# Optimization experiments

Measured on AMD Instinct MI355X. Metric: run time of the kernel, lower is better.

## Reference

```python
import jax, jax.numpy as jnp
import numpy as np

N = 100000   # nodes
E = 256000   # edges
EMB = 300    # emb_dim
L = 5        # num_layer
NUM_BOND_TYPE = 6
NUM_BOND_DIR = 3
BN_EPS = 1e-5


def _bn(h, g, b):
    # BatchNorm1d forward with batch stats (training-mode math, biased var)
    m = jnp.mean(h, axis=0)
    v = jnp.var(h, axis=0)
    return g * (h - m) * jax.lax.rsqrt(v + BN_EPS) + b


def setup_inputs() -> dict:
    key = jax.random.key(0)
    ks = jax.random.split(key, 8)
    x = jax.random.normal(ks[0], (N, EMB), jnp.float32)
    edge_index = jax.random.randint(ks[1], (2, E), 0, N, jnp.int32)
    edge_attr = jax.random.randint(ks[2], (E, 2), 0, 3, jnp.int32)
    # per-layer stacked parameters
    W_bond = jax.random.normal(ks[3], (L, EMB, NUM_BOND_TYPE + NUM_BOND_DIR), jnp.float32) * 0.1
    eps = jnp.zeros((L,), jnp.float32)
    W1 = jax.random.normal(ks[4], (L, 2 * EMB, EMB), jnp.float32) * 0.05
    b1 = jnp.zeros((L, 2 * EMB), jnp.float32)
    bn1_g = jnp.ones((L, 2 * EMB), jnp.float32)
    bn1_b = jnp.zeros((L, 2 * EMB), jnp.float32)
    W2 = jax.random.normal(ks[5], (L, EMB, 2 * EMB), jnp.float32) * 0.05
    b2 = jnp.zeros((L, EMB), jnp.float32)
    bn_g = jnp.ones((L, EMB), jnp.float32)
    bn_b = jnp.zeros((L, EMB), jnp.float32)
    return {"x": x, "W_bond": W_bond, "eps": eps, "W1": W1, "b1": b1,
            "bn1_g": bn1_g, "bn1_b": bn1_b, "W2": W2, "b2": b2,
            "bn_g": bn_g, "bn_b": bn_b,
            "edge_index": edge_index, "edge_attr": edge_attr}


def reference(x, W_bond, eps, W1, b1, bn1_g, bn1_b, W2, b2, bn_g, bn_b,
              edge_index, edge_attr):
    src, dst = edge_index[0], edge_index[1]
    ea0, ea1 = edge_attr[:, 0], edge_attr[:, 1]
    h = x
    for l in range(L):
        # MixedBondEncoder (2-column int branch): two embedding lookups on W.T
        tab = W_bond[l].T  # [9, EMB]
        e = tab[:NUM_BOND_TYPE][ea0] + tab[NUM_BOND_TYPE:][ea1]  # [E, EMB]
        # GIN message: relu(x_j + edge_emb), scatter-add to dst
        msg = jax.nn.relu(h[src] + e)
        agg = jax.ops.segment_sum(msg, dst, num_segments=N)  # [N, EMB]
        z = (1.0 + eps[l]) * h + agg
        # mlp: Linear -> BN -> ReLU -> Linear
        z = z @ W1[l].T + b1[l]
        z = jax.nn.relu(_bn(z, bn1_g[l], bn1_b[l]))
        z = z @ W2[l].T + b2[l]
        # outer BatchNorm, relu except last layer (dropout p=0)
        z = _bn(z, bn_g[l], bn_b[l])
        if l < L - 1:
            z = jax.nn.relu(z)
        h = z
    return h  # JK='last'
```

## Files before the change

kernel.cpp:

```cpp
#include <hip/hip_runtime.h>
#include <hip/hip_bf16.h>
#include <stdint.h>
#include <stddef.h>
#include <string.h>

#define NN 100000
#define NE 256000
#define EMBD 300
#define C1D 600
#define NL 5
#define BNEPS 1e-5f

#define REPBLK 1800

typedef short bf16x8 __attribute__((ext_vector_type(8)));
typedef float f32x4 __attribute__((ext_vector_type(4)));

__device__ __forceinline__ float bf2f(unsigned short u) {
  unsigned int x = ((unsigned int)u) << 16;
  return __uint_as_float(x);
}
__device__ __forceinline__ unsigned short f2bf(float f) {
  unsigned int x = __float_as_uint(f);
  unsigned int r = x + 0x7fffu + ((x >> 16) & 1u);
  return (unsigned short)(r >> 16);
}

__device__ __forceinline__ void split2(float a, float b, unsigned int& hi, unsigned int& lo) {
  float2 p = make_float2(a, b);
  __hip_bfloat162 hb = __float22bfloat162_rn(p);
  unsigned int hraw;
  memcpy(&hraw, &hb, 4);
  float2 hf = __bfloat1622float2(hb);
  float2 lf = make_float2(a - hf.x, b - hf.y);
  __hip_bfloat162 lb = __float22bfloat162_rn(lf);
  unsigned int lraw;
  memcpy(&lraw, &lb, 4);
  hi = hraw; lo = lraw;
}


__global__ void zero_stats_k(float* __restrict__ statrep, int n) {
  int i = blockIdx.x * blockDim.x + threadIdx.x;
  int stride = gridDim.x * blockDim.x;
  for (; i < n; i += stride) statrep[i] = 0.0f;
}

__global__ void preset_ident_k(float* __restrict__ wsf) {
  for (int i = threadIdx.x; i < 300; i += blockDim.x) {
    wsf[1200 + i] = 1.0f;
    wsf[1500 + i] = 0.0f;
  }
}

__global__ void init_agg_k(const float* __restrict__ zin, const float* __restrict__ sc,
                           const float* __restrict__ sh, const float* __restrict__ eps,
                           int l, int relu, float* __restrict__ agg) {
  float s = 1.0f + eps[l];
  int i = blockIdx.x * blockDim.x + threadIdx.x;
  const int n4 = NN * (EMBD / 4);
  if (i >= n4) return;
  int c4 = (i % (EMBD / 4)) * 4;
  float4 v = ((const float4*)zin)[i];
  float4 a = *(const float4*)(sc + c4);
  float4 b = *(const float4*)(sh + c4);
  v.x = v.x * a.x + b.x;
  v.y = v.y * a.y + b.y;
  v.z = v.z * a.z + b.z;
  v.w = v.w * a.w + b.w;
  if (relu) {
    v.x = fmaxf(v.x, 0.0f); v.y = fmaxf(v.y, 0.0f);
    v.z = fmaxf(v.z, 0.0f); v.w = fmaxf(v.w, 0.0f);
  }
  v.x *= s; v.y *= s; v.z *= s; v.w *= s;
  ((float4*)agg)[i] = v;
}

__global__ void edge_scatter_k(const float* __restrict__ zin, const float* __restrict__ Wb_l,
                               const float* __restrict__ sc, const float* __restrict__ sh,
                               int relu,
                               const int* __restrict__ ei, const int* __restrict__ ea,
                               float* __restrict__ agg) {
  __shared__ float tab[EMBD * 9];
  __shared__ float scs[EMBD];
  __shared__ float shs[EMBD];
  for (int i = threadIdx.x; i < EMBD * 9; i += blockDim.x) tab[i] = Wb_l[i];
  for (int i = threadIdx.x; i < EMBD; i += blockDim.x) { scs[i] = sc[i]; shs[i] = sh[i]; }
  __syncthreads();
  int wave = threadIdx.x >> 6;
  int lane = threadIdx.x & 63;
  int e = blockIdx.x * 4 + wave;
  if (e >= NE) return;
  int src = ei[e];
  int dst = ei[NE + e];
  int t0 = ea[2 * e];
  int t1 = ea[2 * e + 1] + 6;
  const float* zs = zin + (size_t)src * EMBD;
  float* ad = agg + (size_t)dst * EMBD;
  for (int d = lane; d < EMBD; d += 64) {
    float hv = zs[d] * scs[d] + shs[d];
    if (relu) hv = fmaxf(hv, 0.0f);
    float m = hv + tab[d * 9 + t0] + tab[d * 9 + t1];
    if (m > 0.0f) atomicAdd(&ad[d], m);
  }
}

__global__ void split_agg_k(unsigned int* __restrict__ a) {
  int i = blockIdx.x * blockDim.x + threadIdx.x;
  const int n4 = NN * (EMBD / 4);
  if (i >= n4) return;
  float4 v = ((const float4*)a)[i];
  unsigned int h0, l0, h1, l1;
  split2(v.x, v.y, h0, l0);
  split2(v.z, v.w, h1, l1);
  uint4 o;
  o.x = __builtin_amdgcn_perm(l0, h0, 0x05040100u);
  o.y = __builtin_amdgcn_perm(l0, h0, 0x07060302u);
  o.z = __builtin_amdgcn_perm(l1, h1, 0x05040100u);
  o.w = __builtin_amdgcn_perm(l1, h1, 0x07060302u);
  ((uint4*)a)[i] = o;
}

__global__ void finalize_k(const float* __restrict__ statrep, int off_sum, int off_sq,
                           int nrep,
                           const float* __restrict__ g, const float* __restrict__ b,
                           float* __restrict__ scale, float* __restrict__ shift, int C) {
  int j = blockIdx.x * blockDim.x + threadIdx.x;
  if (j >= C) return;
  float s = 0.0f, q = 0.0f;
  for (int r = 0; r < nrep; ++r) {
    const float* p = statrep + (size_t)r * REPBLK;
    s += p[off_sum + j];
    q += p[off_sq + j];
  }
  float mean = s * (1.0f / NN);
  float var = q * (1.0f / NN) - mean * mean;
  float sc = g[j] * rsqrtf(var + BNEPS);
  scale[j] = sc;
  shift[j] = b[j] - mean * sc;
}

__global__ void bn_apply_k(const float* __restrict__ z2, const float* __restrict__ scale,
                           const float* __restrict__ shift, int do_relu, float* __restrict__ out) {
  int i = blockIdx.x * blockDim.x + threadIdx.x;
  const int n4 = NN * (EMBD / 4);
  if (i >= n4) return;
  int c4 = (i % (EMBD / 4)) * 4;
  float4 v = ((const float4*)z2)[i];
  float4 sc = *(const float4*)(scale + c4);
  float4 sh = *(const float4*)(shift + c4);
  v.x = v.x * sc.x + sh.x;
  v.y = v.y * sc.y + sh.y;
  v.z = v.z * sc.z + sh.z;
  v.w = v.w * sc.w + sh.w;
  if (do_relu) {
    v.x = fmaxf(v.x, 0.0f); v.y = fmaxf(v.y, 0.0f);
    v.z = fmaxf(v.z, 0.0f); v.w = fmaxf(v.w, 0.0f);
  }
  ((float4*)out)[i] = v;
}


#define TM 128
#define TN 128
#define TK 32
#define LDT 40
#define OTS 136

__global__ __launch_bounds__(256, 2) void gemm1_mfma_k(
    const unsigned int* __restrict__ A,
    const float* __restrict__ W,
    const float* __restrict__ bias,
    unsigned short* __restrict__ Z1,
    float* __restrict__ statrep, int repmask) {
  const int M = NN, K = EMBD, NC = C1D;
  __shared__ unsigned short SM[20480];
  unsigned short* Ah = SM;
  unsigned short* Al = SM + 5120;
  unsigned short* Bh = SM + 10240;
  unsigned short* Bl = SM + 15360;
  unsigned short* OT = SM;

  int tid = threadIdx.x;
  int m0 = blockIdx.x * TM, n0 = blockIdx.y * TN;
  int w = tid >> 6, lane = tid & 63;
  int wm = w & 1, wn = w >> 1;
  int lm16 = lane & 15, quad = lane >> 4;

  f32x4 acc[4][4] = {};

  for (int k0 = 0; k0 < K; k0 += TK) {
#pragma unroll
    for (int i = 0; i < 4; ++i) {
      int u = tid + i * 256;
      int row = u >> 3, q = u & 7;
      int k = k0 + q * 4;
      int m = m0 + row;
      uint4 x = make_uint4(0, 0, 0, 0);
      if (m < M && k + 3 < K) x = *(const uint4*)(A + (size_t)m * K + k);
      unsigned int h01 = __builtin_amdgcn_perm(x.y, x.x, 0x05040100u);
      unsigned int l01 = __builtin_amdgcn_perm(x.y, x.x, 0x07060302u);
      unsigned int h23 = __builtin_amdgcn_perm(x.w, x.z, 0x05040100u);
      unsigned int l23 = __builtin_amdgcn_perm(x.w, x.z, 0x07060302u);
      *(uint2*)&Ah[row * LDT + q * 4] = make_uint2(h01, h23);
      *(uint2*)&Al[row * LDT + q * 4] = make_uint2(l01, l23);
    }
#pragma unroll
    for (int i = 0; i < 4; ++i) {
      int u = tid + i * 256;
      int row = u >> 3, q = u & 7;
      int k = k0 + q * 4;
      int n = n0 + row;
      float4 v = make_float4(0, 0, 0, 0);
      if (n < NC && k + 3 < K) v = *(const float4*)(W + (size_t)n * K + k);
      unsigned int h0, l0, h1, l1;
      split2(v.x, v.y, h0, l0);
      split2(v.z, v.w, h1, l1);
      *(uint2*)&Bh[row * LDT + q * 4] = make_uint2(h0, h1);
      *(uint2*)&Bl[row * LDT + q * 4] = make_uint2(l0, l1);
    }
    __syncthreads();

    bf16x8 ah[4], al[4], bh[4], bl[4];
#pragma unroll
    for (int t = 0; t < 4; ++t) {
      int ar = (wm * 64 + t * 16 + lm16) * LDT + quad * 8;
      ah[t] = *(const bf16x8*)&Ah[ar];
      al[t] = *(const bf16x8*)&Al[ar];
      int br = (wn * 64 + t * 16 + lm16) * LDT + quad * 8;
      bh[t] = *(const bf16x8*)&Bh[br];
      bl[t] = *(const bf16x8*)&Bl[br];
    }
#pragma unroll
    for (int mt = 0; mt < 4; ++mt)
#pragma unroll
      for (int nt = 0; nt < 4; ++nt) {
        acc[mt][nt] = __builtin_amdgcn_mfma_f32_16x16x32_bf16(ah[mt], bh[nt], acc[mt][nt], 0, 0, 0);
        acc[mt][nt] = __builtin_amdgcn_mfma_f32_16x16x32_bf16(al[mt], bh[nt], acc[mt][nt], 0, 0, 0);
        acc[mt][nt] = __builtin_amdgcn_mfma_f32_16x16x32_bf16(ah[mt], bl[nt], acc[mt][nt], 0, 0, 0);
      }
    __syncthreads();
  }

  float* srep = statrep + (size_t)(blockIdx.x & repmask) * REPBLK;

#pragma unroll
  for (int nt = 0; nt < 4; ++nt) {
    int c = n0 + wn * 64 + nt * 16 + lm16;
    bool cv = c < NC;
    float bs = cv ? bias[c] : 0.0f;
    int ocol = wn * 64 + nt * 16 + lm16;
    float csum = 0.0f, csq = 0.0f;
#pragma unroll
    for (int mt = 0; mt < 4; ++mt) {
      int rbase = m0 + wm * 64 + mt * 16 + quad * 4;
      int orow = wm * 64 + mt * 16 + quad * 4;
#pragma unroll
      for (int r = 0; r < 4; ++r) {
        float v = acc[mt][nt][r] + bs;
        OT[(orow + r) * OTS + ocol] = f2bf(v);
        if ((rbase + r) < M && cv) { csum += v; csq += v * v; }
      }
    }
    csum += __shfl_down(csum, 16); csum += __shfl_down(csum, 32);
    csq  += __shfl_down(csq, 16);  csq  += __shfl_down(csq, 32);
    if (quad == 0 && cv) {
      atomicAdd(&srep[c], csum);
      atomicAdd(&srep[600 + c], csq);
    }
  }
  __syncthreads();

  {
    int ncols = NC - n0; if (ncols > TN) ncols = TN;
    int nchunk = ncols >> 3;
    int cc = tid & 15;
    int rr0 = tid >> 4;
    if (cc < nchunk) {
#pragma unroll
      for (int i = 0; i < 8; ++i) {
        int rr = rr0 + i * 16;
        int mm = m0 + rr;
        if (mm < M) {
          uint4 vv = *(const uint4*)&OT[rr * OTS + cc * 8];
          *(uint4*)&Z1[(size_t)mm * NC + n0 + cc * 8] = vv;
        }
      }
    }
  }
}

__global__ __launch_bounds__(256, 2) void gemm2_mfma_k(
    const unsigned short* __restrict__ Z1,
    const float* __restrict__ scale1, const float* __restrict__ shift1,
    const float* __restrict__ W,
    const float* __restrict__ bias,
    float* __restrict__ Z2,
    float* __restrict__ statrep, int repmask) {
  const int M = NN, K = C1D, NC = EMBD;
  __shared__ unsigned short Ah[TM * LDT], Al[TM * LDT];
  __shared__ unsigned short Bh[TN * LDT], Bl[TN * LDT];

  int tid = threadIdx.x;
  int m0 = blockIdx.x * TM, n0 = blockIdx.y * TN;
  int w = tid >> 6, lane = tid & 63;
  int wm = w & 1, wn = w >> 1;
  int lm16 = lane & 15, quad = lane >> 4;

  f32x4 acc[4][4] = {};

  for (int k0 = 0; k0 < K; k0 += TK) {
#pragma unroll
    for (int i = 0; i < 2; ++i) {
      int u = tid + i * 256;
      int row = u >> 2, g = u & 3;
      int k = k0 + g * 8;
      int m = m0 + row;
      float vals[8];
#pragma unroll
      for (int j = 0; j < 8; ++j) vals[j] = 0.0f;
      if (m < M) {
        if (k + 7 < K) {
          union { uint4 u4; unsigned short us[8]; } rr;
          rr.u4 = *(const uint4*)(Z1 + (size_t)m * K + k);
          float4 sc0 = *(const float4*)(scale1 + k);
          float4 sc1 = *(const float4*)(scale1 + k + 4);
          float4 sh0 = *(const float4*)(shift1 + k);
          float4 sh1 = *(const float4*)(shift1 + k + 4);
          const float* scp = &sc0.x; const float* shp = &sh0.x;
          const float* scq = &sc1.x; const float* shq = &sh1.x;
#pragma unroll
          for (int j = 0; j < 4; ++j) {
            vals[j]     = fmaxf(bf2f(rr.us[j])     * scp[j] + shp[j], 0.0f);
            vals[j + 4] = fmaxf(bf2f(rr.us[j + 4]) * scq[j] + shq[j], 0.0f);
          }
        } else {
#pragma unroll
          for (int j = 0; j < 8; ++j) {
            int kk = k + j;
            if (kk < K)
              vals[j] = fmaxf(bf2f(Z1[(size_t)m * K + kk]) * scale1[kk] + shift1[kk], 0.0f);
          }
        }
      }
      unsigned int h[4], l[4];
      split2(vals[0], vals[1], h[0], l[0]);
      split2(vals[2], vals[3], h[1], l[1]);
      split2(vals[4], vals[5], h[2], l[2]);
      split2(vals[6], vals[7], h[3], l[3]);
      *(uint4*)&Ah[row * LDT + g * 8] = make_uint4(h[0], h[1], h[2], h[3]);
      *(uint4*)&Al[row * LDT + g * 8] = make_uint4(l[0], l[1], l[2], l[3]);
    }
#pragma unroll
    for (int i = 0; i < 4; ++i) {
      int u = tid + i * 256;
      int row = u >> 3, q = u & 7;
      int k = k0 + q * 4;
      int n = n0 + row;
      float4 v = make_float4(0, 0, 0, 0);
      if (n < NC) {
        if (k + 3 < K) v = *(const float4*)(W + (size_t)n * K + k);
        else {
          float* vv = &v.x;
#pragma unroll
          for (int j = 0; j < 4; ++j) if (k + j < K) vv[j] = W[(size_t)n * K + k + j];
        }
      }
      unsigned int h0, l0, h1, l1;
      split2(v.x, v.y, h0, l0);
      split2(v.z, v.w, h1, l1);
      *(uint2*)&Bh[row * LDT + q * 4] = make_uint2(h0, h1);
      *(uint2*)&Bl[row * LDT + q * 4] = make_uint2(l0, l1);
    }
    __syncthreads();

    bf16x8 ah[4], al[4], bh[4], bl[4];
#pragma unroll
    for (int t = 0; t < 4; ++t) {
      int ar = (wm * 64 + t * 16 + lm16) * LDT + quad * 8;
      ah[t] = *(const bf16x8*)&Ah[ar];
      al[t] = *(const bf16x8*)&Al[ar];
      int br = (wn * 64 + t * 16 + lm16) * LDT + quad * 8;
      bh[t] = *(const bf16x8*)&Bh[br];
      bl[t] = *(const bf16x8*)&Bl[br];
    }
#pragma unroll
    for (int mt = 0; mt < 4; ++mt)
#pragma unroll
      for (int nt = 0; nt < 4; ++nt) {
        acc[mt][nt] = __builtin_amdgcn_mfma_f32_16x16x32_bf16(ah[mt], bh[nt], acc[mt][nt], 0, 0, 0);
        acc[mt][nt] = __builtin_amdgcn_mfma_f32_16x16x32_bf16(al[mt], bh[nt], acc[mt][nt], 0, 0, 0);
        acc[mt][nt] = __builtin_amdgcn_mfma_f32_16x16x32_bf16(ah[mt], bl[nt], acc[mt][nt], 0, 0, 0);
      }
    __syncthreads();
  }

  float* srep = statrep + (size_t)(blockIdx.x & repmask) * REPBLK;

#pragma unroll
  for (int nt = 0; nt < 4; ++nt) {
    int c = n0 + wn * 64 + nt * 16 + lm16;
    bool cv = c < NC;
    float bs = cv ? bias[c] : 0.0f;
    float csum = 0.0f, csq = 0.0f;
#pragma unroll
    for (int mt = 0; mt < 4; ++mt) {
      int rbase = m0 + wm * 64 + mt * 16 + quad * 4;
#pragma unroll
      for (int r = 0; r < 4; ++r) {
        int mm = rbase + r;
        if (mm < M && cv) {
          float v = acc[mt][nt][r] + bs;
          Z2[(size_t)mm * NC + c] = v;
          csum += v; csq += v * v;
        }
      }
    }
    csum += __shfl_down(csum, 16); csum += __shfl_down(csum, 32);
    csq  += __shfl_down(csq, 16);  csq  += __shfl_down(csq, 32);
    if (quad == 0 && cv) {
      atomicAdd(&srep[1200 + c], csum);
      atomicAdd(&srep[1500 + c], csq);
    }
  }
}


extern "C" void kernel_launch(void* const* d_in, const int* in_sizes, int n_in,
                              void* d_out, int out_size, void* d_ws, size_t ws_size,
                              hipStream_t stream) {
  const float* x    = (const float*)d_in[0];
  const float* Wb   = (const float*)d_in[1];
  const float* eps  = (const float*)d_in[2];
  const float* W1   = (const float*)d_in[3];
  const float* b1   = (const float*)d_in[4];
  const float* bn1g = (const float*)d_in[5];
  const float* bn1b = (const float*)d_in[6];
  const float* W2   = (const float*)d_in[7];
  const float* b2   = (const float*)d_in[8];
  const float* bng  = (const float*)d_in[9];
  const float* bnb  = (const float*)d_in[10];
  const int*   ei   = (const int*)d_in[11];
  const int*   ea   = (const int*)d_in[12];

  float* WS  = (float*)d_ws;
  float* OUT = (float*)d_out;
  float* wsf = (float*)d_ws + (size_t)NN * EMBD;
  float* statrep = wsf + 1800;

  size_t need64 = ((size_t)NN * EMBD + 1800 + (size_t)64 * REPBLK) * sizeof(float);
  int nrep = (ws_size >= need64) ? 64 : 1;
  int repmask = nrep - 1;
  int zn = nrep * REPBLK;

  const int n4 = NN * (EMBD / 4);
  const int eltGrid = (n4 + 255) / 256;

  dim3 g1((NN + TM - 1) / TM, (C1D + TN - 1) / TN);
  dim3 g2((NN + TM - 1) / TM, (EMBD + TN - 1) / TN);

  preset_ident_k<<<1, 256, 0, stream>>>(wsf);

  for (int l = 0; l < NL; ++l) {
    float* aggp = (l & 1) ? OUT : WS;
    float* z1p  = (l & 1) ? WS  : OUT;
    const float* zin = (l == 0) ? x : (const float*)z1p;
    int relu_in = (l > 0) ? 1 : 0;

    zero_stats_k<<<64, 256, 0, stream>>>(statrep, zn);
    init_agg_k<<<eltGrid, 256, 0, stream>>>(zin, wsf + 1200, wsf + 1500, eps, l, relu_in, aggp);
    edge_scatter_k<<<NE / 4, 256, 0, stream>>>(zin, Wb + (size_t)l * EMBD * 9,
                                               wsf + 1200, wsf + 1500, relu_in, ei, ea, aggp);
    split_agg_k<<<eltGrid, 256, 0, stream>>>((unsigned int*)aggp);
    gemm1_mfma_k<<<g1, 256, 0, stream>>>(
        (const unsigned int*)aggp, W1 + (size_t)l * C1D * EMBD, b1 + (size_t)l * C1D,
        (unsigned short*)z1p, statrep, repmask);
    finalize_k<<<3, 256, 0, stream>>>(statrep, 0, 600, nrep, bn1g + (size_t)l * C1D,
                                      bn1b + (size_t)l * C1D, wsf + 0, wsf + 600, C1D);
    gemm2_mfma_k<<<g2, 256, 0, stream>>>(
        (const unsigned short*)z1p, wsf + 0, wsf + 600,
        W2 + (size_t)l * EMBD * C1D, b2 + (size_t)l * EMBD,
        aggp, statrep, repmask);
    finalize_k<<<2, 256, 0, stream>>>(statrep, 1200, 1500, nrep, bng + (size_t)l * EMBD,
                                      bnb + (size_t)l * EMBD, wsf + 1200, wsf + 1500, EMBD);
  }
  bn_apply_k<<<eltGrid, 256, 0, stream>>>(WS, wsf + 1200, wsf + 1500, 0, OUT);
}
```

Measured before the change: 5.341 ms.

## Prefetch next K-tile into registers and swizzle GEMM blocks across XCDs

Both MFMA GEMM kernels now load the next K tile of A and W into registers while the current tile is being multiplied, so global-load latency overlaps with compute. Block indices are also remapped so that blocks sharing an M tile land on the same XCD, which is meant to improve L2 reuse. The remainder-handling branches in gemm2 are simplified because K is divisible by 8. The extra prefetch registers may raise register pressure under the two-blocks-per-CU launch bound.

```diff
diff --git a/kernel.cpp b/kernel.cpp
--- a/kernel.cpp
+++ b/kernel.cpp
@@ -37,6 +37,17 @@
   unsigned int lraw;
   memcpy(&lraw, &lb, 4);
   hi = hraw; lo = lraw;
+}
+
+__device__ __forceinline__ void swizzle_xy(int GX, int GY, int& tx, int& ty) {
+  int nwg = GX * GY;
+  int bid = blockIdx.y * GX + blockIdx.x;
+  int xcd = bid & 7, local = bid >> 3;
+  int q = nwg >> 3, r = nwg & 7;
+  int swz = (xcd < r) ? (xcd * (q + 1) + local)
+                      : (r * (q + 1) + (xcd - r) * q + local);
+  tx = swz / GY;
+  ty = swz - tx * GY;
 }
 
 
@@ -182,44 +193,66 @@
   unsigned short* OT = SM;
 
   int tid = threadIdx.x;
-  int m0 = blockIdx.x * TM, n0 = blockIdx.y * TN;
+  int tx, ty;
+  swizzle_xy(gridDim.x, gridDim.y, tx, ty);
+  int m0 = tx * TM, n0 = ty * TN;
   int w = tid >> 6, lane = tid & 63;
   int wm = w & 1, wn = w >> 1;
   int lm16 = lane & 15, quad = lane >> 4;
+  int srow = tid >> 3, sq = tid & 7;
 
   f32x4 acc[4][4] = {};
+  uint4 pA[4];
+  float4 pB[4];
+
+#pragma unroll
+  for (int i = 0; i < 4; ++i) {
+    int row = srow + i * 32;
+    int k = sq * 4;
+    int m = m0 + row, n = n0 + row;
+    uint4 xa = make_uint4(0, 0, 0, 0);
+    if (m < M && k + 3 < K) xa = *(const uint4*)(A + (size_t)m * K + k);
+    pA[i] = xa;
+    float4 vb = make_float4(0, 0, 0, 0);
+    if (n < NC && k + 3 < K) vb = *(const float4*)(W + (size_t)n * K + k);
+    pB[i] = vb;
+  }
 
   for (int k0 = 0; k0 < K; k0 += TK) {
 #pragma unroll
     for (int i = 0; i < 4; ++i) {
-      int u = tid + i * 256;
-      int row = u >> 3, q = u & 7;
-      int k = k0 + q * 4;
-      int m = m0 + row;
-      uint4 x = make_uint4(0, 0, 0, 0);
-      if (m < M && k + 3 < K) x = *(const uint4*)(A + (size_t)m * K + k);
+      int row = srow + i * 32;
+      uint4 x = pA[i];
       unsigned int h01 = __builtin_amdgcn_perm(x.y, x.x, 0x05040100u);
       unsigned int l01 = __builtin_amdgcn_perm(x.y, x.x, 0x07060302u);
       unsigned int h23 = __builtin_amdgcn_perm(x.w, x.z, 0x05040100u);
       unsigned int l23 = __builtin_amdgcn_perm(x.w, x.z, 0x07060302u);
-      *(uint2*)&Ah[row * LDT + q * 4] = make_uint2(h01, h23);
-      *(uint2*)&Al[row * LDT + q * 4] = make_uint2(l01, l23);
-    }
-#pragma unroll
-    for (int i = 0; i < 4; ++i) {
-      int u = tid + i * 256;
-      int row = u >> 3, q = u & 7;
-      int k = k0 + q * 4;
-      int n = n0 + row;
-      float4 v = make_float4(0, 0, 0, 0);
-      if (n < NC && k + 3 < K) v = *(const float4*)(W + (size_t)n * K + k);
-      unsigned int h0, l0, h1, l1;
-      split2(v.x, v.y, h0, l0);
-      split2(v.z, v.w, h1, l1);
-      *(uint2*)&Bh[row * LDT + q * 4] = make_uint2(h0, h1);
-      *(uint2*)&Bl[row * LDT + q * 4] = make_uint2(l0, l1);
+      *(uint2*)&Ah[row * LDT + sq * 4] = make_uint2(h01, h23);
+      *(uint2*)&Al[row * LDT + sq * 4] = make_uint2(l01, l23);
+      float4 v = pB[i];
+      unsigned int bh0, bl0, bh1, bl1;
+      split2(v.x, v.y, bh0, bl0);
+      split2(v.z, v.w, bh1, bl1);
+      *(uint2*)&Bh[row * LDT + sq * 4] = make_uint2(bh0, bh1);
+      *(uint2*)&Bl[row * LDT + sq * 4] = make_uint2(bl0, bl1);
     }
     __syncthreads();
+
+    if (k0 + TK < K) {
+      int kn = k0 + TK;
+#pragma unroll
+      for (int i = 0; i < 4; ++i) {
+        int row = srow + i * 32;
+        int k = kn + sq * 4;
+        int m = m0 + row, n = n0 + row;
+        uint4 xa = make_uint4(0, 0, 0, 0);
+        if (m < M && k + 3 < K) xa = *(const uint4*)(A + (size_t)m * K + k);
+        pA[i] = xa;
+        float4 vb = make_float4(0, 0, 0, 0);
+        if (n < NC && k + 3 < K) vb = *(const float4*)(W + (size_t)n * K + k);
+        pB[i] = vb;
+      }
+    }
 
     bf16x8 ah[4], al[4], bh[4], bl[4];
 #pragma unroll
@@ -302,45 +335,60 @@
   __shared__ unsigned short Bh[TN * LDT], Bl[TN * LDT];
 
   int tid = threadIdx.x;
-  int m0 = blockIdx.x * TM, n0 = blockIdx.y * TN;
+  int tx, ty;
+  swizzle_xy(gridDim.x, gridDim.y, tx, ty);
+  int m0 = tx * TM, n0 = ty * TN;
   int w = tid >> 6, lane = tid & 63;
   int wm = w & 1, wn = w >> 1;
   int lm16 = lane & 15, quad = lane >> 4;
+  int arow = tid >> 2, ag = tid & 3;
+  int brow = tid >> 3, bq = tid & 7;
 
   f32x4 acc[4][4] = {};
+  uint4 pA[2];
+  float4 pB[4];
+
+#pragma unroll
+  for (int i = 0; i < 2; ++i) {
+    int row = arow + i * 64;
+    int k = ag * 8;
+    int m = m0 + row;
+    uint4 xa = make_uint4(0, 0, 0, 0);
+    if (m < M && k + 7 < K) xa = *(const uint4*)(Z1 + (size_t)m * K + k);
+    pA[i] = xa;
+  }
+#pragma unroll
+  for (int i = 0; i < 4; ++i) {
+    int row = brow + i * 32;
+    int k = bq * 4;
+    int n = n0 + row;
+    float4 vb = make_float4(0, 0, 0, 0);
+    if (n < NC && k + 3 < K) vb = *(const float4*)(W + (size_t)n * K + k);
+    pB[i] = vb;
+  }
 
   for (int k0 = 0; k0 < K; k0 += TK) {
 #pragma unroll
     for (int i = 0; i < 2; ++i) {
-      int u = tid + i * 256;
-      int row = u >> 2, g = u & 3;
-      int k = k0 + g * 8;
+      int row = arow + i * 64;
+      int k = k0 + ag * 8;
       int m = m0 + row;
       float vals[8];
 #pragma unroll
       for (int j = 0; j < 8; ++j) vals[j] = 0.0f;
-      if (m < M) {
-        if (k + 7 < K) {
-          union { uint4 u4; unsigned short us[8]; } rr;
-          rr.u4 = *(const uint4*)(Z1 + (size_t)m * K + k);
-          float4 sc0 = *(const float4*)(scale1 + k);
-          float4 sc1 = *(const float4*)(scale1 + k + 4);
-          float4 sh0 = *(const float4*)(shift1 + k);
-          float4 sh1 = *(const float4*)(shift1 + k + 4);
-          const float* scp = &sc0.x; const float* shp = &sh0.x;
-          const float* scq = &sc1.x; const float* shq = &sh1.x;
-#pragma unroll
-          for (int j = 0; j < 4; ++j) {
-            vals[j]     = fmaxf(bf2f(rr.us[j])     * scp[j] + shp[j], 0.0f);
-            vals[j + 4] = fmaxf(bf2f(rr.us[j + 4]) * scq[j] + shq[j], 0.0f);
-          }
-        } else {
-#pragma unroll
-          for (int j = 0; j < 8; ++j) {
-            int kk = k + j;
-            if (kk < K)
-              vals[j] = fmaxf(bf2f(Z1[(size_t)m * K + kk]) * scale1[kk] + shift1[kk], 0.0f);
-          }
+      if (m < M && k + 7 < K) {
+        union { uint4 u4; unsigned short us[8]; } rr;
+        rr.u4 = pA[i];
+        float4 sc0 = *(const float4*)(scale1 + k);
+        float4 sc1 = *(const float4*)(scale1 + k + 4);
+        float4 sh0 = *(const float4*)(shift1 + k);
+        float4 sh1 = *(const float4*)(shift1 + k + 4);
+        const float* scp = &sc0.x; const float* shp = &sh0.x;
+        const float* scq = &sc1.x; const float* shq = &sh1.x;
+#pragma unroll
+        for (int j = 0; j < 4; ++j) {
+          vals[j]     = fmaxf(bf2f(rr.us[j])     * scp[j] + shp[j], 0.0f);
+          vals[j + 4] = fmaxf(bf2f(rr.us[j + 4]) * scq[j] + shq[j], 0.0f);
         }
       }
       unsigned int h[4], l[4];
@@ -348,31 +396,42 @@
       split2(vals[2], vals[3], h[1], l[1]);
       split2(vals[4], vals[5], h[2], l[2]);
       split2(vals[6], vals[7], h[3], l[3]);
-      *(uint4*)&Ah[row * LDT + g * 8] = make_uint4(h[0], h[1], h[2], h[3]);
-      *(uint4*)&Al[row * LDT + g * 8] = make_uint4(l[0], l[1], l[2], l[3]);
+      *(uint4*)&Ah[row * LDT + ag * 8] = make_uint4(h[0], h[1], h[2], h[3]);
+      *(uint4*)&Al[row * LDT + ag * 8] = make_uint4(l[0], l[1], l[2], l[3]);
     }
 #pragma unroll
     for (int i = 0; i < 4; ++i) {
-      int u = tid + i * 256;
-      int row = u >> 3, q = u & 7;
-      int k = k0 + q * 4;
-      int n = n0 + row;
-      float4 v = make_float4(0, 0, 0, 0);
-      if (n < NC) {
-        if (k + 3 < K) v = *(const float4*)(W + (size_t)n * K + k);
-        else {
-          float* vv = &v.x;
-#pragma unroll
-          for (int j = 0; j < 4; ++j) if (k + j < K) vv[j] = W[(size_t)n * K + k + j];
-        }
-      }
+      int row = brow + i * 32;
+      float4 v = pB[i];
       unsigned int h0, l0, h1, l1;
       split2(v.x, v.y, h0, l0);
       split2(v.z, v.w, h1, l1);
-      *(uint2*)&Bh[row * LDT + q * 4] = make_uint2(h0, h1);
-      *(uint2*)&Bl[row * LDT + q * 4] = make_uint2(l0, l1);
+      *(uint2*)&Bh[row * LDT + bq * 4] = make_uint2(h0, h1);
+      *(uint2*)&Bl[row * LDT + bq * 4] = make_uint2(l0, l1);
     }
     __syncthreads();
+
+    if (k0 + TK < K) {
+      int kn = k0 + TK;
+#pragma unroll
+      for (int i = 0; i < 2; ++i) {
+        int row = arow + i * 64;
+        int k = kn + ag * 8;
+        int m = m0 + row;
+        uint4 xa = make_uint4(0, 0, 0, 0);
+        if (m < M && k + 7 < K) xa = *(const uint4*)(Z1 + (size_t)m * K + k);
+        pA[i] = xa;
+      }
+#pragma unroll
+      for (int i = 0; i < 4; ++i) {
+        int row = brow + i * 32;
+        int k = kn + bq * 4;
+        int n = n0 + row;
+        float4 vb = make_float4(0, 0, 0, 0);
+        if (n < NC && k + 3 < K) vb = *(const float4*)(W + (size_t)n * K + k);
+        pB[i] = vb;
+      }
+    }
 
     bf16x8 ah[4], al[4], bh[4], bl[4];
 #pragma unroll
```

After: 4.700 ms. -12.0%, faster.
